# Optimization experiments

Hardware: AMD Instinct MI355X
Metric: run time of the kernel (lower is better)

Reference implementation:

```python
import jax, jax.numpy as jnp
import numpy as np

DIM = 256
HEADS = 8
WS = 7
MLP_HIDDEN = int(DIM * 2.0)
LN_EPS = 1e-5


def _ln(x, g, b):
    m = x.mean(-1, keepdims=True)
    v = ((x - m) ** 2).mean(-1, keepdims=True)
    return (x - m) / jnp.sqrt(v + LN_EPS) * g + b


def setup_inputs() -> dict:
    key = jax.random.key(0)
    ks = jax.random.split(key, 6)
    B, H, W, C = 32, 56, 56, DIM
    s = lambda k, shape: jax.random.normal(k, shape, jnp.float32) * 0.02
    return {
        "x": jax.random.normal(ks[0], (B, H * W, C), jnp.float32),
        "H": H,
        "W": W,
        "norm1_g": jnp.ones((C,), jnp.float32),
        "norm1_b": jnp.zeros((C,), jnp.float32),
        "in_proj_w": s(ks[1], (3 * C, C)),
        "in_proj_b": jnp.zeros((3 * C,), jnp.float32),
        "out_proj_w": s(ks[2], (C, C)),
        "out_proj_b": jnp.zeros((C,), jnp.float32),
        "norm2_g": jnp.ones((C,), jnp.float32),
        "norm2_b": jnp.zeros((C,), jnp.float32),
        "mlp_w1": s(ks[3], (MLP_HIDDEN, C)),
        "mlp_b1": jnp.zeros((MLP_HIDDEN,), jnp.float32),
        "mlp_w2": s(ks[4], (C, MLP_HIDDEN)),
        "mlp_b2": jnp.zeros((C,), jnp.float32),
    }


def reference(x, H, W, norm1_g, norm1_b, in_proj_w, in_proj_b, out_proj_w,
              out_proj_b, norm2_g, norm2_b, mlp_w1, mlp_b1, mlp_w2, mlp_b2):
    B, N, C = x.shape
    ws = WS
    shortcut = x

    h = _ln(x, norm1_g, norm1_b).reshape(B, H, W, C)  # channels-last (equiv. math)
    pad_h = (ws - H % ws) % ws
    pad_w = (ws - W % ws) % ws
    h = jnp.pad(h, ((0, 0), (0, pad_h), (0, pad_w), (0, 0)), mode="reflect")
    Hp, Wp = H + pad_h, W + pad_w
    nh, nw = Hp // ws, Wp // ws

    # window partition -> (B*nh*nw, ws*ws, C)
    h = h.reshape(B, nh, ws, nw, ws, C).transpose(0, 1, 3, 2, 4, 5)
    h = h.reshape(B * nh * nw, ws * ws, C)

    # torch nn.MultiheadAttention (batch_first), q=k=v=h
    hd = C // HEADS
    qkv = h @ in_proj_w.T + in_proj_b               # (Bw, L, 3C)
    q, k, v = jnp.split(qkv, 3, axis=-1)
    Bw, L, _ = q.shape
    q = q.reshape(Bw, L, HEADS, hd).transpose(0, 2, 1, 3)
    k = k.reshape(Bw, L, HEADS, hd).transpose(0, 2, 1, 3)
    v = v.reshape(Bw, L, HEADS, hd).transpose(0, 2, 1, 3)
    scores = jnp.einsum("bhqd,bhkd->bhqk", q, k) / jnp.sqrt(jnp.float32(hd))
    attn = jax.nn.softmax(scores, axis=-1)
    o = jnp.einsum("bhqk,bhkd->bhqd", attn, v)
    o = o.transpose(0, 2, 1, 3).reshape(Bw, L, C)
    o = o @ out_proj_w.T + out_proj_b

    # window merge, crop padding
    o = o.reshape(B, nh, nw, ws, ws, C).transpose(0, 1, 3, 2, 4, 5)
    o = o.reshape(B, Hp, Wp, C)[:, :H, :W, :].reshape(B, N, C)

    x = shortcut + o
    h2 = _ln(x, norm2_g, norm2_b)
    h2 = jax.nn.gelu(h2 @ mlp_w1.T + mlp_b1, approximate=False) @ mlp_w2.T + mlp_b2
    return x + h2
```

## Files before the change

kernel.cpp:

```cpp
#include <hip/hip_runtime.h>
#include <hip/hip_bf16.h>
#include <math.h>

#define NTOK 3136
#define C_ 256
#define HEADS_ 8
#define HD 32
#define WS_ 7
#define L_ 49
#define NWIN 2048
#define NWH 16384
#define M_ 100352
#define MLPH 512
#define WHSZ 2048

typedef __bf16 bf16x8 __attribute__((ext_vector_type(8)));
typedef float f32x4 __attribute__((ext_vector_type(4)));

__device__ __forceinline__ unsigned short f2bf(float f) {
    union { float f; unsigned u; } v; v.f = f;
    unsigned r = v.u + 0x7fffu + ((v.u >> 16) & 1u);
    return (unsigned short)(r >> 16);
}
__device__ __forceinline__ float bf2f(unsigned short s) {
    union { unsigned u; float f; } v; v.u = ((unsigned)s) << 16;
    return v.f;
}

__device__ __forceinline__ int t2rr(int t) {
    int win = t / L_;
    int l   = t - win * L_;
    int b_  = win >> 6, wh = (win >> 3) & 7, ww = win & 7;
    int ld7 = l / WS_;
    int y   = wh * WS_ + ld7;
    int xc  = ww * WS_ + (l - ld7 * WS_);
    return b_ * NTOK + y * 56 + xc;
}

template <int NBN>
__device__ __forceinline__ void xcd_decode(int nb, int& bm, int& bn) {
    int h = blockIdx.x;
    int fid = (h & 7) * (nb >> 3) + (h >> 3);
    int bmi = fid / NBN;
    bm = bmi * 128;
    bn = (fid - bmi * NBN) * 128;
}

__global__ __launch_bounds__(256) void cvt_kernel(
    const float* __restrict__ in, unsigned short* __restrict__ out, int n)
{
    int i = blockIdx.x * 256 + threadIdx.x;
    if (i < n) out[i] = f2bf(in[i]);
}

__global__ __launch_bounds__(256) void ln_kernel(
    const float* __restrict__ x, const float* __restrict__ gamma,
    const float* __restrict__ beta, unsigned short* __restrict__ out)
{
    int wave = threadIdx.x >> 6;
    int lane = threadIdx.x & 63;
    int p = blockIdx.x * 4 + wave;
    const float* row = x + (size_t)p * C_;
    float4 v = *(const float4*)(row + lane * 4);
    float s  = v.x + v.y + v.z + v.w;
    float ss = v.x * v.x + v.y * v.y + v.z * v.z + v.w * v.w;
    #pragma unroll
    for (int m = 1; m < 64; m <<= 1) {
        s  += __shfl_xor(s, m, 64);
        ss += __shfl_xor(ss, m, 64);
    }
    float mean = s * (1.0f / C_);
    float var  = ss * (1.0f / C_) - mean * mean;
    float inv  = rsqrtf(var + 1e-5f);
    float4 gv = *(const float4*)(gamma + lane * 4);
    float4 bv = *(const float4*)(beta + lane * 4);
    int b_ = p / NTOK, n = p - b_ * NTOK;
    int y = n / 56, xc = n - y * 56;
    int win = (b_ * 8 + y / WS_) * 8 + xc / WS_;
    int l   = (y % WS_) * WS_ + (xc % WS_);
    size_t orow = (size_t)(win * L_ + l) * C_;
    unsigned short o[4];
    o[0] = f2bf((v.x - mean) * inv * gv.x + bv.x);
    o[1] = f2bf((v.y - mean) * inv * gv.y + bv.y);
    o[2] = f2bf((v.z - mean) * inv * gv.z + bv.z);
    o[3] = f2bf((v.w - mean) * inv * gv.w + bv.w);
    *(uint2*)(out + orow + lane * 4) = *(const uint2*)o;
}

#define GBM 128
#define GBN 128
#define GBK 32

__device__ __forceinline__ void gload_lds16(const void* g, void* l) {
    __builtin_amdgcn_global_load_lds(
        (const __attribute__((address_space(1))) unsigned*)g,
        (__attribute__((address_space(3))) unsigned*)l, 16, 0, 0);
}

template <int EPI, int NBN>
__global__ __launch_bounds__(256) void mgemm(
    const unsigned short* __restrict__ A, const unsigned short* __restrict__ W,
    const float* __restrict__ bias, void* __restrict__ outv,
    int M, int N, int K)
{
    __shared__ __align__(16) unsigned short As[GBM * GBK];
    __shared__ __align__(16) unsigned short Bs[GBN * GBK];

    int tid  = threadIdx.x;
    int w    = tid >> 6;
    int lane = tid & 63;
    int wr = w >> 1, wc = w & 1;
    int bm, bn;
    xcd_decode<NBN>(gridDim.x, bm, bn);
    int srow = lane >> 2;
    int scol = (lane & 3) * 8;
    int c = lane & 15, hi = lane >> 4;

    f32x4 acc[4][4] = {};

    for (int k0 = 0; k0 < K; k0 += GBK) {
        #pragma unroll
        for (int i = 0; i < 2; ++i) {
            int ra = w * 32 + i * 16;
            gload_lds16(A + (size_t)(bm + ra + srow) * K + k0 + scol, &As[ra * GBK]);
            gload_lds16(W + (size_t)(bn + ra + srow) * K + k0 + scol, &Bs[ra * GBK]);
        }
        __syncthreads();

        bf16x8 af[4], bf[4];
        #pragma unroll
        for (int mi = 0; mi < 4; ++mi)
            af[mi] = *(const bf16x8*)&As[(wr * 64 + mi * 16 + c) * GBK + hi * 8];
        #pragma unroll
        for (int ni = 0; ni < 4; ++ni)
            bf[ni] = *(const bf16x8*)&Bs[(wc * 64 + ni * 16 + c) * GBK + hi * 8];

        #pragma unroll
        for (int mi = 0; mi < 4; ++mi)
            #pragma unroll
            for (int ni = 0; ni < 4; ++ni)
                acc[mi][ni] = __builtin_amdgcn_mfma_f32_16x16x32_bf16(
                    af[mi], bf[ni], acc[mi][ni], 0, 0, 0);
        __syncthreads();
    }

    #pragma unroll
    for (int mi = 0; mi < 4; ++mi) {
        #pragma unroll
        for (int r = 0; r < 4; ++r) {
            int row = bm + wr * 64 + mi * 16 + hi * 4 + r;
            int win, l;
            if (EPI == 0) { win = row / L_; l = row - win * L_; }
            #pragma unroll
            for (int ni = 0; ni < 4; ++ni) {
                int col = bn + wc * 64 + ni * 16 + c;
                float val = acc[mi][ni][r] + bias[col];
                if (EPI == 0) {
                    int which = col >> 8;
                    int head  = (col >> 5) & 7;
                    int d     = col & 31;
                    int wh = win * HEADS_ + head;
                    size_t base = (size_t)which * ((size_t)NWH * WHSZ) + (size_t)wh * WHSZ;
                    size_t off;
                    if (which == 2)
                        off = base + (size_t)(((l >> 3) * HD + d) << 3) + (l & 7);
                    else
                        off = base + (size_t)l * HD + d;
                    ((unsigned short*)outv)[off] = f2bf(val);
                } else {
                    float g = 0.5f * val * (1.0f + erff(val * 0.70710678118654752f));
                    ((unsigned short*)outv)[(size_t)row * N + col] = f2bf(g);
                }
            }
        }
    }
}

__global__ __launch_bounds__(512) void mgemm_ln(
    const unsigned short* __restrict__ A, const unsigned short* __restrict__ W,
    const float* __restrict__ bias, const float* __restrict__ x,
    const float* __restrict__ g2, const float* __restrict__ b2,
    unsigned short* __restrict__ x1_out, unsigned short* __restrict__ ln_out)
{
    __shared__ __align__(16) unsigned short As[128 * 32];
    __shared__ __align__(16) unsigned short Bs[256 * 32];
    __shared__ __align__(16) unsigned short X1s[128][256];

    int tid  = threadIdx.x;
    int w    = tid >> 6;
    int lane = tid & 63;
    int wr = w >> 2, wc = w & 3;
    int bm = blockIdx.x * 128;
    int srow = lane >> 2;
    int scol = (lane & 3) * 8;
    int c = lane & 15, hi = lane >> 4;

    f32x4 acc[4][4] = {};

    for (int k0 = 0; k0 < 256; k0 += 32) {
        gload_lds16(A + (size_t)(bm + w * 16 + srow) * 256 + k0 + scol,
                    &As[(w * 16) * 32]);
        #pragma unroll
        for (int i = 0; i < 2; ++i) {
            int ra = w * 32 + i * 16;
            gload_lds16(W + (size_t)(ra + srow) * 256 + k0 + scol, &Bs[ra * 32]);
        }
        __syncthreads();

        bf16x8 af[4], bf[4];
        #pragma unroll
        for (int mi = 0; mi < 4; ++mi)
            af[mi] = *(const bf16x8*)&As[(wr * 64 + mi * 16 + c) * 32 + hi * 8];
        #pragma unroll
        for (int ni = 0; ni < 4; ++ni)
            bf[ni] = *(const bf16x8*)&Bs[(wc * 64 + ni * 16 + c) * 32 + hi * 8];

        #pragma unroll
        for (int mi = 0; mi < 4; ++mi)
            #pragma unroll
            for (int ni = 0; ni < 4; ++ni)
                acc[mi][ni] = __builtin_amdgcn_mfma_f32_16x16x32_bf16(
                    af[mi], bf[ni], acc[mi][ni], 0, 0, 0);
        __syncthreads();
    }

    #pragma unroll
    for (int mi = 0; mi < 4; ++mi) {
        #pragma unroll
        for (int ni = 0; ni < 4; ++ni) {
            int colb = wc * 64 + ni * 16 + c;
            float bv = bias[colb];
            #pragma unroll
            for (int r = 0; r < 4; ++r)
                X1s[wr * 64 + mi * 16 + hi * 4 + r][colb] = f2bf(acc[mi][ni][r] + bv);
        }
    }
    __syncthreads();

    float4 gv = *(const float4*)(g2 + lane * 4);
    float4 bv2 = *(const float4*)(b2 + lane * 4);
    #pragma unroll 2
    for (int i = 0; i < 16; ++i) {
        int tl = w * 16 + i;
        int t = bm + tl;
        int rr = t2rr(t);
        float4 xv = *(const float4*)(x + (size_t)rr * C_ + lane * 4);
        uint2 ov = *(const uint2*)&X1s[tl][lane * 4];
        float x0 = xv.x + bf2f(ov.x & 0xffff);
        float x1 = xv.y + bf2f(ov.x >> 16);
        float x2 = xv.z + bf2f(ov.y & 0xffff);
        float x3 = xv.w + bf2f(ov.y >> 16);
        float s  = x0 + x1 + x2 + x3;
        float ss = x0 * x0 + x1 * x1 + x2 * x2 + x3 * x3;
        #pragma unroll
        for (int m = 1; m < 64; m <<= 1) {
            s  += __shfl_xor(s, m, 64);
            ss += __shfl_xor(ss, m, 64);
        }
        float mean = s * (1.0f / C_);
        float var  = ss * (1.0f / C_) - mean * mean;
        float inv  = rsqrtf(var + 1e-5f);
        uint2 xw, lw;
        xw.x = (unsigned)f2bf(x0) | ((unsigned)f2bf(x1) << 16);
        xw.y = (unsigned)f2bf(x2) | ((unsigned)f2bf(x3) << 16);
        float l0 = (x0 - mean) * inv * gv.x + bv2.x;
        float l1 = (x1 - mean) * inv * gv.y + bv2.y;
        float l2 = (x2 - mean) * inv * gv.z + bv2.z;
        float l3 = (x3 - mean) * inv * gv.w + bv2.w;
        lw.x = (unsigned)f2bf(l0) | ((unsigned)f2bf(l1) << 16);
        lw.y = (unsigned)f2bf(l2) | ((unsigned)f2bf(l3) << 16);
        *(uint2*)(x1_out + (size_t)t * C_ + lane * 4) = xw;
        *(uint2*)(ln_out + (size_t)t * C_ + lane * 4) = lw;
    }
}

__global__ __launch_bounds__(256) void mgemm_out(
    const unsigned short* __restrict__ A, const unsigned short* __restrict__ W,
    const float* __restrict__ bias, const unsigned short* __restrict__ x1,
    float* __restrict__ dout)
{
    __shared__ __align__(16) unsigned short lds_pool[8192];
    unsigned short* As = lds_pool;
    unsigned short* Bs = lds_pool + 4096;
    float* stage = (float*)lds_pool;

    int tid  = threadIdx.x;
    int w    = tid >> 6;
    int lane = tid & 63;
    int wr = w >> 1, wc = w & 1;
    int bm, bn;
    xcd_decode<2>(gridDim.x, bm, bn);
    int srow = lane >> 2;
    int scol = (lane & 3) * 8;
    int c = lane & 15, hi = lane >> 4;

    f32x4 acc[4][4] = {};

    for (int k0 = 0; k0 < 512; k0 += 32) {
        #pragma unroll
        for (int i = 0; i < 2; ++i) {
            int ra = w * 32 + i * 16;
            gload_lds16(A + (size_t)(bm + ra + srow) * 512 + k0 + scol, &As[ra * 32]);
            gload_lds16(W + (size_t)(bn + ra + srow) * 512 + k0 + scol, &Bs[ra * 32]);
        }
        __syncthreads();

        bf16x8 af[4], bf[4];
        #pragma unroll
        for (int mi = 0; mi < 4; ++mi)
            af[mi] = *(const bf16x8*)&As[(wr * 64 + mi * 16 + c) * 32 + hi * 8];
        #pragma unroll
        for (int ni = 0; ni < 4; ++ni)
            bf[ni] = *(const bf16x8*)&Bs[(wc * 64 + ni * 16 + c) * 32 + hi * 8];

        #pragma unroll
        for (int mi = 0; mi < 4; ++mi)
            #pragma unroll
            for (int ni = 0; ni < 4; ++ni)
                acc[mi][ni] = __builtin_amdgcn_mfma_f32_16x16x32_bf16(
                    af[mi], bf[ni], acc[mi][ni], 0, 0, 0);
        __syncthreads();
    }

    #pragma unroll
    for (int c2 = 0; c2 < 4; ++c2) {
        if (wr == (c2 >> 1)) {
            int mi0 = (c2 & 1) * 2;
            #pragma unroll
            for (int mm = 0; mm < 2; ++mm) {
                #pragma unroll
                for (int ni = 0; ni < 4; ++ni) {
                    int colb = wc * 64 + ni * 16 + c;
                    float bv = bias[bn + colb];
                    #pragma unroll
                    for (int r = 0; r < 4; ++r)
                        stage[(mm * 16 + hi * 4 + r) * 128 + colb] =
                            acc[mi0 + mm][ni][r] + bv;
                }
            }
        }
        __syncthreads();
        #pragma unroll
        for (int i = 0; i < 4; ++i) {
            int lr = i * 8 + (tid >> 5);
            int t = bm + c2 * 32 + lr;
            int rr = t2rr(t);
            int col4 = (tid & 31) * 4;
            float4 v = *(const float4*)&stage[lr * 128 + col4];
            uint2 rv = *(const uint2*)&x1[(size_t)t * C_ + bn + col4];
            v.x += bf2f(rv.x & 0xffff);
            v.y += bf2f(rv.x >> 16);
            v.z += bf2f(rv.y & 0xffff);
            v.w += bf2f(rv.y >> 16);
            *(float4*)&dout[(size_t)rr * C_ + bn + col4] = v;
        }
        __syncthreads();
    }
}

__global__ __launch_bounds__(256) void mattn(
    const unsigned short* __restrict__ qkv, unsigned short* __restrict__ o_win)
{
    __shared__ __align__(16) unsigned short P_lds[4][64][72];
    int wave = threadIdx.x >> 6, lane = threadIdx.x & 63;
    int c = lane & 15, hi = lane >> 4;
    int wh = blockIdx.x * 4 + wave;
    int win = wh >> 3, head = wh & 7;
    const unsigned short* qb = qkv + (size_t)wh * WHSZ;
    const unsigned short* kb = qb + (size_t)NWH * WHSZ;
    const unsigned short* vb = kb + (size_t)NWH * WHSZ;

    bf16x8 af[4], bk[4];
    #pragma unroll
    for (int mi = 0; mi < 4; ++mi)
        af[mi] = *(const bf16x8*)(qb + (mi * 16 + c) * HD + hi * 8);
    #pragma unroll
    for (int ni = 0; ni < 4; ++ni)
        bk[ni] = *(const bf16x8*)(kb + (ni * 16 + c) * HD + hi * 8);

    f32x4 sacc[4][4] = {};
    #pragma unroll
    for (int mi = 0; mi < 4; ++mi)
        #pragma unroll
        for (int ni = 0; ni < 4; ++ni)
            sacc[mi][ni] = __builtin_amdgcn_mfma_f32_16x16x32_bf16(
                af[mi], bk[ni], sacc[mi][ni], 0, 0, 0);

    const float scale = 0.17677669529663687f;
    float inv_[4][4];
    #pragma unroll
    for (int mi = 0; mi < 4; ++mi) {
        #pragma unroll
        for (int r = 0; r < 4; ++r) {
            float sv[4];
            float m = -1e30f;
            #pragma unroll
            for (int ni = 0; ni < 4; ++ni) {
                float v = sacc[mi][ni][r] * scale;
                v = (ni * 16 + c < L_) ? v : -1e30f;
                sv[ni] = v;
                m = fmaxf(m, v);
            }
            #pragma unroll
            for (int msk = 1; msk < 16; msk <<= 1)
                m = fmaxf(m, __shfl_xor(m, msk, 64));
            float sum = 0.f;
            unsigned short pb[4];
            #pragma unroll
            for (int ni = 0; ni < 4; ++ni) {
                float p = __expf(sv[ni] - m);
                sum += p;
                pb[ni] = f2bf(p);
            }
            #pragma unroll
            for (int msk = 1; msk < 16; msk <<= 1)
                sum += __shfl_xor(sum, msk, 64);
            inv_[mi][r] = 1.0f / sum;
            int q = mi * 16 + hi * 4 + r;
            #pragma unroll
            for (int ni = 0; ni < 4; ++ni)
                P_lds[wave][q][ni * 16 + c] = pb[ni];
        }
    }

    f32x4 oacc[4][2] = {};
    #pragma unroll
    for (int ks = 0; ks < 2; ++ks) {
        bf16x8 pa[4], bv[2];
        #pragma unroll
        for (int mi = 0; mi < 4; ++mi)
            pa[mi] = *(const bf16x8*)&P_lds[wave][mi * 16 + c][ks * 32 + hi * 8];
        #pragma unroll
        for (int ni = 0; ni < 2; ++ni)
            bv[ni] = *(const bf16x8*)(vb + ((ks * 4 + hi) * HD + ni * 16 + c) * 8);
        #pragma unroll
        for (int mi = 0; mi < 4; ++mi)
            #pragma unroll
            for (int ni = 0; ni < 2; ++ni)
                oacc[mi][ni] = __builtin_amdgcn_mfma_f32_16x16x32_bf16(
                    pa[mi], bv[ni], oacc[mi][ni], 0, 0, 0);
    }

    #pragma unroll
    for (int mi = 0; mi < 4; ++mi) {
        #pragma unroll
        for (int r = 0; r < 4; ++r) {
            int q = mi * 16 + hi * 4 + r;
            if (q < L_) {
                size_t rowoff = ((size_t)(win * L_ + q)) * C_ + head * HD;
                float iv = inv_[mi][r];
                #pragma unroll
                for (int ni = 0; ni < 2; ++ni)
                    o_win[rowoff + ni * 16 + c] = f2bf(oacc[mi][ni][r] * iv);
            }
        }
    }
}

extern "C" void kernel_launch(void* const* d_in, const int* in_sizes, int n_in,
                              void* d_out, int out_size, void* d_ws, size_t ws_size,
                              hipStream_t stream)
{
    (void)in_sizes; (void)n_in; (void)out_size; (void)ws_size;
    const float* x    = (const float*)d_in[0];
    const float* n1g  = (const float*)d_in[3];
    const float* n1b  = (const float*)d_in[4];
    const float* wqkv = (const float*)d_in[5];
    const float* bqkv = (const float*)d_in[6];
    const float* wout = (const float*)d_in[7];
    const float* bout = (const float*)d_in[8];
    const float* n2g  = (const float*)d_in[9];
    const float* n2b  = (const float*)d_in[10];
    const float* w1   = (const float*)d_in[11];
    const float* b1   = (const float*)d_in[12];
    const float* w2   = (const float*)d_in[13];
    const float* b2   = (const float*)d_in[14];
    float* out = (float*)d_out;

    unsigned short* bufA_bf = (unsigned short*)d_ws;
    unsigned short* qkv_bf  = bufA_bf + (size_t)M_ * C_;
    unsigned short* x1_bf   = qkv_bf + (size_t)3 * NWH * WHSZ;
    unsigned short* ln2_bf  = x1_bf + (size_t)M_ * C_;
    unsigned short* wqkv_bf = ln2_bf + (size_t)M_ * C_;
    unsigned short* wout_bf = wqkv_bf + 768 * 256;
    unsigned short* w1_bf   = wout_bf + 256 * 256;
    unsigned short* w2_bf   = w1_bf + 512 * 256;

    cvt_kernel<<<(768 * 256 + 255) / 256, 256, 0, stream>>>(wqkv, wqkv_bf, 768 * 256);
    cvt_kernel<<<(256 * 256 + 255) / 256, 256, 0, stream>>>(wout, wout_bf, 256 * 256);
    cvt_kernel<<<(512 * 256 + 255) / 256, 256, 0, stream>>>(w1, w1_bf, 512 * 256);
    cvt_kernel<<<(256 * 512 + 255) / 256, 256, 0, stream>>>(w2, w2_bf, 256 * 512);

    ln_kernel<<<M_ / 4, 256, 0, stream>>>(x, n1g, n1b, bufA_bf);

    mgemm<0, 6><<<(M_ / GBM) * 6, 256, 0, stream>>>(
        bufA_bf, wqkv_bf, bqkv, qkv_bf, M_, 3 * C_, C_);

    mattn<<<NWH / 4, 256, 0, stream>>>(qkv_bf, bufA_bf);

    mgemm_ln<<<M_ / 128, 512, 0, stream>>>(
        bufA_bf, wout_bf, bout, x, n2g, n2b, x1_bf, ln2_bf);

    mgemm<2, 4><<<(M_ / GBM) * 4, 256, 0, stream>>>(
        ln2_bf, w1_bf, b1, qkv_bf, M_, MLPH, C_);

    mgemm_out<<<(M_ / 128) * 2, 256, 0, stream>>>(
        qkv_bf, w2_bf, b2, x1_bf, out);
}
```

Measured before the change: 423.4 us.

## Double-buffer LDS tiles with XOR swizzle and pad epilogue staging in GEMMs

The three MFMA GEMM kernels now use two LDS buffers, so the global-to-LDS load of the next K tile is issued before the current tile's MFMAs and only one barrier is needed per step. The LDS column offset gets an XOR swizzle on both the load side and the fragment-read side to cut bank conflicts. The epilogue staging arrays are padded (row strides 260 and 132) for the same reason. The extra buffers raise LDS use per block, which may lower occupancy, and the swizzle indexing has to match exactly between writes and reads.

```diff
diff --git a/kernel.cpp b/kernel.cpp
--- a/kernel.cpp
+++ b/kernel.cpp
@@ -103,8 +103,8 @@
     const float* __restrict__ bias, void* __restrict__ outv,
     int M, int N, int K)
 {
-    __shared__ __align__(16) unsigned short As[GBM * GBK];
-    __shared__ __align__(16) unsigned short Bs[GBN * GBK];
+    __shared__ __align__(16) unsigned short As0[GBM * GBK], As1[GBM * GBK];
+    __shared__ __align__(16) unsigned short Bs0[GBN * GBK], Bs1[GBN * GBK];
 
     int tid  = threadIdx.x;
     int w    = tid >> 6;
@@ -113,35 +113,56 @@
     int bm, bn;
     xcd_decode<NBN>(gridDim.x, bm, bn);
     int srow = lane >> 2;
-    int scol = (lane & 3) * 8;
+    int scol = ((lane & 3) ^ ((lane >> 3) & 3)) * 8;
     int c = lane & 15, hi = lane >> 4;
+    int hs = (hi ^ ((c >> 1) & 3)) * 8;
 
     f32x4 acc[4][4] = {};
 
-    for (int k0 = 0; k0 < K; k0 += GBK) {
+    auto stage = [&](unsigned short* asd, unsigned short* bsd, int k0) {
         #pragma unroll
         for (int i = 0; i < 2; ++i) {
             int ra = w * 32 + i * 16;
-            gload_lds16(A + (size_t)(bm + ra + srow) * K + k0 + scol, &As[ra * GBK]);
-            gload_lds16(W + (size_t)(bn + ra + srow) * K + k0 + scol, &Bs[ra * GBK]);
-        }
-        __syncthreads();
-
-        bf16x8 af[4], bf[4];
-        #pragma unroll
-        for (int mi = 0; mi < 4; ++mi)
-            af[mi] = *(const bf16x8*)&As[(wr * 64 + mi * 16 + c) * GBK + hi * 8];
+            gload_lds16(A + (size_t)(bm + ra + srow) * K + k0 + scol, asd + ra * GBK);
+            gload_lds16(W + (size_t)(bn + ra + srow) * K + k0 + scol, bsd + ra * GBK);
+        }
+    };
+    auto frags = [&](const unsigned short* asd, const unsigned short* bsd,
+                     bf16x8* af, bf16x8* bf) {
+        #pragma unroll
+        for (int mi = 0; mi < 4; ++mi)
+            af[mi] = *(const bf16x8*)&asd[(wr * 64 + mi * 16 + c) * GBK + hs];
         #pragma unroll
         for (int ni = 0; ni < 4; ++ni)
-            bf[ni] = *(const bf16x8*)&Bs[(wc * 64 + ni * 16 + c) * GBK + hi * 8];
-
+            bf[ni] = *(const bf16x8*)&bsd[(wc * 64 + ni * 16 + c) * GBK + hs];
+    };
+    auto domfma = [&](bf16x8* af, bf16x8* bf) {
         #pragma unroll
         for (int mi = 0; mi < 4; ++mi)
             #pragma unroll
             for (int ni = 0; ni < 4; ++ni)
                 acc[mi][ni] = __builtin_amdgcn_mfma_f32_16x16x32_bf16(
                     af[mi], bf[ni], acc[mi][ni], 0, 0, 0);
-        __syncthreads();
+    };
+
+    int NT = K / GBK;
+    stage(As0, Bs0, 0);
+    __syncthreads();
+    for (int t = 0; t < NT; t += 2) {
+        {
+            bf16x8 af[4], bf[4];
+            frags(As0, Bs0, af, bf);
+            if (t + 1 < NT) stage(As1, Bs1, (t + 1) * GBK);
+            domfma(af, bf);
+            __syncthreads();
+        }
+        if (t + 1 < NT) {
+            bf16x8 af[4], bf[4];
+            frags(As1, Bs1, af, bf);
+            if (t + 2 < NT) stage(As0, Bs0, (t + 2) * GBK);
+            domfma(af, bf);
+            __syncthreads();
+        }
     }
 
     #pragma unroll
@@ -176,15 +197,19 @@
     }
 }
 
+#define XS 260
+
 __global__ __launch_bounds__(512) void mgemm_ln(
     const unsigned short* __restrict__ A, const unsigned short* __restrict__ W,
     const float* __restrict__ bias, const float* __restrict__ x,
     const float* __restrict__ g2, const float* __restrict__ b2,
     unsigned short* __restrict__ x1_out, unsigned short* __restrict__ ln_out)
 {
-    __shared__ __align__(16) unsigned short As[128 * 32];
-    __shared__ __align__(16) unsigned short Bs[256 * 32];
-    __shared__ __align__(16) unsigned short X1s[128][256];
+    __shared__ __align__(16) unsigned short pool[128 * XS];
+    unsigned short* As0 = pool;
+    unsigned short* As1 = pool + 4096;
+    unsigned short* Bs0 = pool + 8192;
+    unsigned short* Bs1 = pool + 16384;
 
     int tid  = threadIdx.x;
     int w    = tid >> 6;
@@ -192,36 +217,56 @@
     int wr = w >> 2, wc = w & 3;
     int bm = blockIdx.x * 128;
     int srow = lane >> 2;
-    int scol = (lane & 3) * 8;
+    int scol = ((lane & 3) ^ ((lane >> 3) & 3)) * 8;
     int c = lane & 15, hi = lane >> 4;
+    int hs = (hi ^ ((c >> 1) & 3)) * 8;
 
     f32x4 acc[4][4] = {};
 
-    for (int k0 = 0; k0 < 256; k0 += 32) {
+    auto stage = [&](unsigned short* asd, unsigned short* bsd, int k0) {
         gload_lds16(A + (size_t)(bm + w * 16 + srow) * 256 + k0 + scol,
-                    &As[(w * 16) * 32]);
+                    asd + (w * 16) * 32);
         #pragma unroll
         for (int i = 0; i < 2; ++i) {
             int ra = w * 32 + i * 16;
-            gload_lds16(W + (size_t)(ra + srow) * 256 + k0 + scol, &Bs[ra * 32]);
-        }
-        __syncthreads();
-
-        bf16x8 af[4], bf[4];
-        #pragma unroll
-        for (int mi = 0; mi < 4; ++mi)
-            af[mi] = *(const bf16x8*)&As[(wr * 64 + mi * 16 + c) * 32 + hi * 8];
+            gload_lds16(W + (size_t)(ra + srow) * 256 + k0 + scol, bsd + ra * 32);
+        }
+    };
+    auto frags = [&](const unsigned short* asd, const unsigned short* bsd,
+                     bf16x8* af, bf16x8* bf) {
+        #pragma unroll
+        for (int mi = 0; mi < 4; ++mi)
+            af[mi] = *(const bf16x8*)&asd[(wr * 64 + mi * 16 + c) * 32 + hs];
         #pragma unroll
         for (int ni = 0; ni < 4; ++ni)
-            bf[ni] = *(const bf16x8*)&Bs[(wc * 64 + ni * 16 + c) * 32 + hi * 8];
-
+            bf[ni] = *(const bf16x8*)&bsd[(wc * 64 + ni * 16 + c) * 32 + hs];
+    };
+    auto domfma = [&](bf16x8* af, bf16x8* bf) {
         #pragma unroll
         for (int mi = 0; mi < 4; ++mi)
             #pragma unroll
             for (int ni = 0; ni < 4; ++ni)
                 acc[mi][ni] = __builtin_amdgcn_mfma_f32_16x16x32_bf16(
                     af[mi], bf[ni], acc[mi][ni], 0, 0, 0);
-        __syncthreads();
+    };
+
+    stage(As0, Bs0, 0);
+    __syncthreads();
+    for (int t = 0; t < 8; t += 2) {
+        {
+            bf16x8 af[4], bf[4];
+            frags(As0, Bs0, af, bf);
+            stage(As1, Bs1, (t + 1) * 32);
+            domfma(af, bf);
+            __syncthreads();
+        }
+        {
+            bf16x8 af[4], bf[4];
+            frags(As1, Bs1, af, bf);
+            if (t + 2 < 8) stage(As0, Bs0, (t + 2) * 32);
+            domfma(af, bf);
+            __syncthreads();
+        }
     }
 
     #pragma unroll
@@ -232,7 +277,8 @@
             float bv = bias[colb];
             #pragma unroll
             for (int r = 0; r < 4; ++r)
-                X1s[wr * 64 + mi * 16 + hi * 4 + r][colb] = f2bf(acc[mi][ni][r] + bv);
+                pool[(wr * 64 + mi * 16 + hi * 4 + r) * XS + colb] =
+                    f2bf(acc[mi][ni][r] + bv);
         }
     }
     __syncthreads();
@@ -245,7 +291,7 @@
         int t = bm + tl;
         int rr = t2rr(t);
         float4 xv = *(const float4*)(x + (size_t)rr * C_ + lane * 4);
-        uint2 ov = *(const uint2*)&X1s[tl][lane * 4];
+        uint2 ov = *(const uint2*)&pool[tl * XS + lane * 4];
         float x0 = xv.x + bf2f(ov.x & 0xffff);
         float x1 = xv.y + bf2f(ov.x >> 16);
         float x2 = xv.z + bf2f(ov.y & 0xffff);
@@ -279,10 +325,12 @@
     const float* __restrict__ bias, const unsigned short* __restrict__ x1,
     float* __restrict__ dout)
 {
-    __shared__ __align__(16) unsigned short lds_pool[8192];
-    unsigned short* As = lds_pool;
-    unsigned short* Bs = lds_pool + 4096;
-    float* stage = (float*)lds_pool;
+    __shared__ __align__(16) unsigned short pool[16384];
+    unsigned short* As0 = pool;
+    unsigned short* As1 = pool + 4096;
+    unsigned short* Bs0 = pool + 8192;
+    unsigned short* Bs1 = pool + 12288;
+    float* stg = (float*)pool;
 
     int tid  = threadIdx.x;
     int w    = tid >> 6;
@@ -291,35 +339,55 @@
     int bm, bn;
     xcd_decode<2>(gridDim.x, bm, bn);
     int srow = lane >> 2;
-    int scol = (lane & 3) * 8;
+    int scol = ((lane & 3) ^ ((lane >> 3) & 3)) * 8;
     int c = lane & 15, hi = lane >> 4;
+    int hs = (hi ^ ((c >> 1) & 3)) * 8;
 
     f32x4 acc[4][4] = {};
 
-    for (int k0 = 0; k0 < 512; k0 += 32) {
+    auto stage = [&](unsigned short* asd, unsigned short* bsd, int k0) {
         #pragma unroll
         for (int i = 0; i < 2; ++i) {
             int ra = w * 32 + i * 16;
-            gload_lds16(A + (size_t)(bm + ra + srow) * 512 + k0 + scol, &As[ra * 32]);
-            gload_lds16(W + (size_t)(bn + ra + srow) * 512 + k0 + scol, &Bs[ra * 32]);
-        }
-        __syncthreads();
-
-        bf16x8 af[4], bf[4];
-        #pragma unroll
-        for (int mi = 0; mi < 4; ++mi)
-            af[mi] = *(const bf16x8*)&As[(wr * 64 + mi * 16 + c) * 32 + hi * 8];
+            gload_lds16(A + (size_t)(bm + ra + srow) * 512 + k0 + scol, asd + ra * 32);
+            gload_lds16(W + (size_t)(bn + ra + srow) * 512 + k0 + scol, bsd + ra * 32);
+        }
+    };
+    auto frags = [&](const unsigned short* asd, const unsigned short* bsd,
+                     bf16x8* af, bf16x8* bf) {
+        #pragma unroll
+        for (int mi = 0; mi < 4; ++mi)
+            af[mi] = *(const bf16x8*)&asd[(wr * 64 + mi * 16 + c) * 32 + hs];
         #pragma unroll
         for (int ni = 0; ni < 4; ++ni)
-            bf[ni] = *(const bf16x8*)&Bs[(wc * 64 + ni * 16 + c) * 32 + hi * 8];
-
+            bf[ni] = *(const bf16x8*)&bsd[(wc * 64 + ni * 16 + c) * 32 + hs];
+    };
+    auto domfma = [&](bf16x8* af, bf16x8* bf) {
         #pragma unroll
         for (int mi = 0; mi < 4; ++mi)
             #pragma unroll
             for (int ni = 0; ni < 4; ++ni)
                 acc[mi][ni] = __builtin_amdgcn_mfma_f32_16x16x32_bf16(
                     af[mi], bf[ni], acc[mi][ni], 0, 0, 0);
-        __syncthreads();
+    };
+
+    stage(As0, Bs0, 0);
+    __syncthreads();
+    for (int t = 0; t < 16; t += 2) {
+        {
+            bf16x8 af[4], bf[4];
+            frags(As0, Bs0, af, bf);
+            stage(As1, Bs1, (t + 1) * 32);
+            domfma(af, bf);
+            __syncthreads();
+        }
+        {
+            bf16x8 af[4], bf[4];
+            frags(As1, Bs1, af, bf);
+            if (t + 2 < 16) stage(As0, Bs0, (t + 2) * 32);
+            domfma(af, bf);
+            __syncthreads();
+        }
     }
 
     #pragma unroll
@@ -334,7 +402,7 @@
                     float bv = bias[bn + colb];
                     #pragma unroll
                     for (int r = 0; r < 4; ++r)
-                        stage[(mm * 16 + hi * 4 + r) * 128 + colb] =
+                        stg[(mm * 16 + hi * 4 + r) * 132 + colb] =
                             acc[mi0 + mm][ni][r] + bv;
                 }
             }
@@ -346,7 +414,7 @@
             int t = bm + c2 * 32 + lr;
             int rr = t2rr(t);
             int col4 = (tid & 31) * 4;
-            float4 v = *(const float4*)&stage[lr * 128 + col4];
+            float4 v = *(const float4*)&stg[lr * 132 + col4];
             uint2 rv = *(const uint2*)&x1[(size_t)t * C_ + bn + col4];
             v.x += bf2f(rv.x & 0xffff);
             v.y += bf2f(rv.x >> 16);
```

Result: slower. 434.0 us (+2.5%).
